# Kernel optimization log

Measured on AMD Instinct MI355X. Metric: run time of the kernel, lower is better.

The kernel has to match this reference:

```python
import jax, jax.numpy as jnp
import numpy as np

DIM = 192
HEADS = 6
WIN = 7
N = WIN * WIN            # 49 tokens per window
NW = 64                  # windows per image
B = 64                   # images
BW = NW * B              # 4096 total windows
TABLE = (2 * WIN - 1) ** 2  # 169


def setup_inputs() -> dict:
    key = jax.random.key(0)
    ks = jax.random.split(key, 8)
    x = jax.random.normal(ks[0], (BW, N, DIM), dtype=jnp.float32)
    rpi = jax.random.randint(ks[1], (N, N), 0, TABLE, dtype=jnp.int64)
    # 0 / -100 additive mask (as in shifted-window attention)
    mask = jnp.where(jax.random.uniform(ks[2], (NW, N, N)) < 0.1, -100.0, 0.0).astype(jnp.float32)
    qkv_w = jax.random.normal(ks[3], (3 * DIM, DIM), dtype=jnp.float32) * 0.02
    qkv_b = jnp.zeros((3 * DIM,), dtype=jnp.float32)
    proj_w = jax.random.normal(ks[4], (DIM, DIM), dtype=jnp.float32) * 0.02
    proj_b = jnp.zeros((DIM,), dtype=jnp.float32)
    rpb_table = jax.random.normal(ks[5], (TABLE, HEADS), dtype=jnp.float32) * 0.02
    return {"x": x, "rpi": rpi, "mask": mask, "qkv_w": qkv_w, "qkv_b": qkv_b,
            "proj_w": proj_w, "proj_b": proj_b, "rpb_table": rpb_table}


def reference(x, rpi, mask, qkv_w, qkv_b, proj_w, proj_b, rpb_table):
    b_, n, c = x.shape
    hd = c // HEADS
    scale = hd ** -0.5
    qkv = (x @ qkv_w.T + qkv_b).reshape(b_, n, 3, HEADS, hd)
    qkv = jnp.transpose(qkv, (2, 0, 3, 1, 4))
    q, k, v = qkv[0], qkv[1], qkv[2]
    attn = jnp.einsum('bhnd,bhmd->bhnm', q * scale, k)  # [b_, h, n, n]
    # relative position bias gather: [n, n, h] -> [h, n, n]
    bias = rpb_table[rpi.reshape(-1)].reshape(n, n, HEADS)
    attn = attn + jnp.transpose(bias, (2, 0, 1))[None]
    # additive 0/-inf window mask
    nw = mask.shape[0]
    attn = attn.reshape(b_ // nw, nw, HEADS, n, n) + mask[None, :, None]
    attn = attn.reshape(-1, HEADS, n, n)
    attn = jax.nn.softmax(attn, axis=-1)
    out = jnp.einsum('bhnm,bhmd->bhnd', attn, v)
    out = jnp.transpose(out, (0, 2, 1, 3)).reshape(b_, n, c)
    out = out @ proj_w.T + proj_b
    return out
```

## Files before the change

kernel.cpp:

```cpp
#include <hip/hip_runtime.h>

#define DIM    192
#define HEADS  6
#define NTOK   49
#define NWIN   64

typedef __attribute__((ext_vector_type(8))) short short8;
typedef __attribute__((ext_vector_type(4))) float f32x4;

#define XS 200
#define VS 72
#define SS 65
#define PS 72

#define BIAS_ELEMS (HEADS * NTOK * NTOK)
#define WQKV_SOFF   28864
#define WQKV_ELEMS  (3 * DIM * DIM)
#define WPROJ_SOFF  (WQKV_SOFF + WQKV_ELEMS)
#define WPROJ_ELEMS (DIM * DIM)
#define CMB_BOFF    ((size_t)(WPROJ_SOFF + WPROJ_ELEMS) * 2)
#define CMB_ELEMS   (NWIN * HEADS * NTOK * NTOK)

__device__ __forceinline__ unsigned short f2bf(float f) {
    unsigned int u = __float_as_uint(f);
    u += 0x7FFFu + ((u >> 16) & 1u);
    return (unsigned short)(u >> 16);
}

__global__ void wa_prep_kernel(const int* __restrict__ rpi,
                               const float* __restrict__ rpb,
                               const float* __restrict__ qkv_w,
                               const float* __restrict__ proj_w,
                               const float* __restrict__ maskp,
                               float* __restrict__ bias,
                               unsigned short* __restrict__ wqkv,
                               unsigned short* __restrict__ wproj,
                               float* __restrict__ cmb) {
    __shared__ int is64_s;
    if (threadIdx.x < 64) {
        int z = (rpi[2 * (int)threadIdx.x + 1] == 0) ? 1 : 0;
        unsigned long long b = __ballot(z);
        if (threadIdx.x == 0) is64_s = (__popcll(b) >= 48) ? 1 : 0;
    }
    __syncthreads();
    const int is64 = is64_s;
    const int base3 = BIAS_ELEMS + WQKV_ELEMS + WPROJ_ELEMS;
    const int total = base3 + (cmb ? CMB_ELEMS : 0);
    for (int idx = blockIdx.x * blockDim.x + threadIdx.x; idx < total;
         idx += gridDim.x * blockDim.x) {
        if (idx < BIAS_ELEMS) {
            int h  = idx / (NTOK * NTOK);
            int nm = idx - h * (NTOK * NTOK);
            int r  = is64 ? rpi[2 * nm] : rpi[nm];
            bias[idx] = rpb[r * HEADS + h];
        } else if (idx < BIAS_ELEMS + WQKV_ELEMS) {
            int i = idx - BIAS_ELEMS;
            wqkv[i] = f2bf(qkv_w[i]);
        } else if (idx < base3) {
            int i = idx - BIAS_ELEMS - WQKV_ELEMS;
            wproj[i] = f2bf(proj_w[i]);
        } else {
            int i2  = idx - base3;
            int win = i2 / (HEADS * NTOK * NTOK);
            int rem = i2 - win * (HEADS * NTOK * NTOK);
            int h   = rem / (NTOK * NTOK);
            int nm  = rem - h * (NTOK * NTOK);
            int r   = is64 ? rpi[2 * nm] : rpi[nm];
            cmb[i2] = rpb[r * HEADS + h] + maskp[win * (NTOK * NTOK) + nm];
        }
    }
}

template <bool CMB>
__global__ __launch_bounds__(512, 4)
void wa_attn_kernel(const float* __restrict__ x,
                    const float* __restrict__ maskp,
                    const unsigned short* __restrict__ wqkv,
                    const float* __restrict__ qkv_b,
                    const float* __restrict__ biasp,
                    const unsigned short* __restrict__ wproj,
                    const float* __restrict__ proj_b,
                    const float* __restrict__ cmbp,
                    float* __restrict__ out) {
    __shared__ __attribute__((aligned(16))) float uSP[64 * SS + 64 * (PS / 2)];
    __shared__ __attribute__((aligned(16))) unsigned short sq[64 * XS];
    __shared__ __attribute__((aligned(16))) unsigned short sv[DIM * VS];
    __shared__ float sinv[64];

    unsigned short* sx     = (unsigned short*)uSP;
    unsigned short* kstage = (unsigned short*)uSP;
    float* S = uSP;
    unsigned short* P = (unsigned short*)(uSP + 64 * SS);

    const int tid  = threadIdx.x;
    const int wave = tid >> 6;
    const int lane = tid & 63;
    const int quad = lane >> 4;
    const int l16  = lane & 15;
    const int bw   = blockIdx.x;
    const int win  = bw & (NWIN - 1);

    {
        const float4* xw = (const float4*)(x + (size_t)bw * (NTOK * DIM));
        for (int idx = tid; idx < NTOK * DIM / 4; idx += 512) {
            int row = idx / 48, c4 = idx - row * 48;
            float4 v = xw[idx];
            unsigned int lo = (unsigned int)f2bf(v.x) | ((unsigned int)f2bf(v.y) << 16);
            unsigned int hi = (unsigned int)f2bf(v.z) | ((unsigned int)f2bf(v.w) << 16);
            *(uint2*)&sx[row * XS + c4 * 4] = make_uint2(lo, hi);
        }
        for (int idx = tid; idx < 15 * 24; idx += 512) {
            int row = 49 + idx / 24, c8 = idx - (idx / 24) * 24;
            *(uint4*)&sx[row * XS + c8 * 8] = make_uint4(0, 0, 0, 0);
        }
    }
    __syncthreads();

    {
        const int wm = wave >> 2;
        const int wn = wave & 3;
        #pragma unroll
        for (int cc = 0; cc < 3; ++cc) {
            const int c = (cc == 0) ? 0 : (cc == 1 ? 2 : 1);
            f32x4 acc[3][2];
            #pragma unroll
            for (int r = 0; r < 3; ++r)
                #pragma unroll
                for (int mi = 0; mi < 2; ++mi) acc[r][mi] = (f32x4){0.f, 0.f, 0.f, 0.f};
            for (int k0 = 0; k0 < DIM; k0 += 32) {
                short8 af[2];
                #pragma unroll
                for (int mi = 0; mi < 2; ++mi)
                    af[mi] = *(const short8*)&sx[((wm * 2 + mi) * 16 + l16) * XS + k0 + quad * 8];
                #pragma unroll
                for (int r = 0; r < 3; ++r) {
                    int n0 = c * 192 + (wn + 4 * r) * 16;
                    short8 bf = *(const short8*)(wqkv + (n0 + l16) * DIM + k0 + quad * 8);
                    #pragma unroll
                    for (int mi = 0; mi < 2; ++mi)
                        acc[r][mi] = __builtin_amdgcn_mfma_f32_16x16x32_bf16(af[mi], bf, acc[r][mi], 0, 0, 0);
                }
            }
            if (c == 1) __syncthreads();
            #pragma unroll
            for (int r = 0; r < 3; ++r) {
                int ccol = (wn + 4 * r) * 16 + l16;
                float cb = qkv_b[c * 192 + ccol];
                #pragma unroll
                for (int mi = 0; mi < 2; ++mi) {
                    int mbase = (wm * 2 + mi) * 16 + quad * 4;
                    if (c == 2) {
                        unsigned int lo = (unsigned int)f2bf(acc[r][mi][0] + cb) |
                                          ((unsigned int)f2bf(acc[r][mi][1] + cb) << 16);
                        unsigned int hi = (unsigned int)f2bf(acc[r][mi][2] + cb) |
                                          ((unsigned int)f2bf(acc[r][mi][3] + cb) << 16);
                        *(uint2*)&sv[ccol * VS + mbase] = make_uint2(lo, hi);
                    } else if (c == 1) {
                        #pragma unroll
                        for (int rr = 0; rr < 4; ++rr)
                            kstage[(mbase + rr) * XS + ccol] = f2bf(acc[r][mi][rr] + cb);
                    } else {
                        #pragma unroll
                        for (int rr = 0; rr < 4; ++rr)
                            sq[(mbase + rr) * XS + ccol] = f2bf(acc[r][mi][rr] + cb);
                    }
                }
            }
        }
    }
    __syncthreads();

    short8 kf[2][HEADS];
    #pragma unroll
    for (int tt = 0; tt < 2; ++tt) {
        int t = wave * 2 + tt, nt = t & 3;
        #pragma unroll
        for (int h = 0; h < HEADS; ++h)
            kf[tt][h] = *(const short8*)&kstage[(nt * 16 + l16) * XS + h * 32 + quad * 8];
    }
    __syncthreads();

    const float scale = 0.17677669529663687f;
    const float* maskw = maskp + win * (NTOK * NTOK);

    #pragma unroll
    for (int h = 0; h < HEADS; ++h) {
        {
            f32x4 zz = {0.f, 0.f, 0.f, 0.f};
            const float* cw = CMB ? (cmbp + ((size_t)win * HEADS + h) * (NTOK * NTOK))
                                  : (biasp + h * (NTOK * NTOK));
            #pragma unroll
            for (int tt = 0; tt < 2; ++tt) {
                int t = wave * 2 + tt;
                int mt = t >> 2, nt = t & 3;
                short8 af = *(const short8*)&sq[(mt * 16 + l16) * XS + h * 32 + quad * 8];
                f32x4 d = __builtin_amdgcn_mfma_f32_16x16x32_bf16(af, kf[tt][h], zz, 0, 0, 0);
                #pragma unroll
                for (int rr = 0; rr < 4; ++rr) {
                    int i = mt * 16 + quad * 4 + rr;
                    int j = nt * 16 + l16;
                    if (i < NTOK && j < NTOK) {
                        float add = CMB ? cw[i * NTOK + j]
                                        : (cw[i * NTOK + j] + maskw[i * NTOK + j]);
                        S[i * SS + j] = d[rr] * scale + add;
                    }
                }
            }
        }
        __syncthreads();
        if (tid < 392) {
            int i = tid >> 3, s = tid & 7;
            float m = -1e30f;
            for (int jj = 0; jj < 7; ++jj) {
                int j = s + 8 * jj;
                if (j < NTOK) m = fmaxf(m, S[i * SS + j]);
            }
            for (int o = 1; o < 8; o <<= 1) m = fmaxf(m, __shfl_xor(m, o));
            float sum = 0.f;
            #pragma unroll
            for (int jj = 0; jj < 8; ++jj) {
                int j = s + 8 * jj;
                float e = 0.f;
                if (j < NTOK) { e = __expf(S[i * SS + j] - m); sum += e; }
                P[i * PS + j] = f2bf(e);
            }
            for (int o = 1; o < 8; o <<= 1) sum += __shfl_xor(sum, o);
            if (s == 0) sinv[i] = 1.f / sum;
        }
        __syncthreads();
        {
            int mt = wave >> 1, nt = wave & 1;
            f32x4 acc = {0.f, 0.f, 0.f, 0.f};
            #pragma unroll
            for (int k0 = 0; k0 < 64; k0 += 32) {
                short8 af = *(const short8*)&P[(mt * 16 + l16) * PS + k0 + quad * 8];
                short8 bf = *(const short8*)&sv[(h * 32 + nt * 16 + l16) * VS + k0 + quad * 8];
                acc = __builtin_amdgcn_mfma_f32_16x16x32_bf16(af, bf, acc, 0, 0, 0);
            }
            #pragma unroll
            for (int rr = 0; rr < 4; ++rr) {
                int i = mt * 16 + quad * 4 + rr;
                unsigned short ov = 0;
                if (i < NTOK) ov = f2bf(acc[rr] * sinv[i]);
                sq[i * XS + h * 32 + nt * 16 + l16] = ov;
            }
        }
    }
    __syncthreads();

    {
        const int mh = wave >> 2;
        const int wv = wave & 3;
        f32x4 pacc[3][2];
        #pragma unroll
        for (int r = 0; r < 3; ++r)
            #pragma unroll
            for (int mi = 0; mi < 2; ++mi) pacc[r][mi] = (f32x4){0.f, 0.f, 0.f, 0.f};
        for (int k0 = 0; k0 < DIM; k0 += 32) {
            short8 af[2];
            #pragma unroll
            for (int mi = 0; mi < 2; ++mi)
                af[mi] = *(const short8*)&sq[((mh * 2 + mi) * 16 + l16) * XS + k0 + quad * 8];
            #pragma unroll
            for (int r = 0; r < 3; ++r) {
                int n0 = (wv + 4 * r) * 16;
                short8 bf = *(const short8*)(wproj + (n0 + l16) * DIM + k0 + quad * 8);
                #pragma unroll
                for (int mi = 0; mi < 2; ++mi)
                    pacc[r][mi] = __builtin_amdgcn_mfma_f32_16x16x32_bf16(af[mi], bf, pacc[r][mi], 0, 0, 0);
            }
        }
        #pragma unroll
        for (int r = 0; r < 3; ++r) {
            int n0 = (wv + 4 * r) * 16;
            float cb = proj_b[n0 + l16];
            #pragma unroll
            for (int mi = 0; mi < 2; ++mi) {
                #pragma unroll
                for (int rr = 0; rr < 4; ++rr) {
                    int m = (mh * 2 + mi) * 16 + quad * 4 + rr;
                    if (m < NTOK)
                        out[((size_t)bw * NTOK + m) * DIM + n0 + l16] = pacc[r][mi][rr] + cb;
                }
            }
        }
    }
}

extern "C" void kernel_launch(void* const* d_in, const int* in_sizes, int n_in,
                              void* d_out, int out_size, void* d_ws, size_t ws_size,
                              hipStream_t stream) {
    const float* x      = (const float*)d_in[0];
    const int*   rpi    = (const int*)d_in[1];
    const float* maskp  = (const float*)d_in[2];
    const float* qkv_w  = (const float*)d_in[3];
    const float* qkv_b  = (const float*)d_in[4];
    const float* proj_w = (const float*)d_in[5];
    const float* proj_b = (const float*)d_in[6];
    const float* rpb    = (const float*)d_in[7];
    float* out = (float*)d_out;

    float* bias = (float*)d_ws;
    unsigned short* wqkv  = (unsigned short*)d_ws + WQKV_SOFF;
    unsigned short* wproj = (unsigned short*)d_ws + WPROJ_SOFF;
    float* cmb = nullptr;
    if (ws_size >= CMB_BOFF + (size_t)CMB_ELEMS * 4)
        cmb = (float*)((char*)d_ws + CMB_BOFF);

    wa_prep_kernel<<<640, 256, 0, stream>>>(rpi, rpb, qkv_w, proj_w, maskp,
                                            bias, wqkv, wproj, cmb);
    if (cmb)
        wa_attn_kernel<true><<<4096, 512, 0, stream>>>(x, maskp, wqkv, qkv_b, bias,
                                                       wproj, proj_b, cmb, out);
    else
        wa_attn_kernel<false><<<4096, 512, 0, stream>>>(x, maskp, wqkv, qkv_b, bias,
                                                        wproj, proj_b, cmb, out);
}
```

Measured before the change: 629.7 us.

## Keep softmax in registers and overlap PV of previous head with QK

Computes S^T = K·Q^T per query tile so each lane holds a query's scores in registers, doing max/sum via cross-quad shuffles instead of an LDS score buffer and a separate softmax pass. Waves 0-3 do QK+softmax for head h while waves 4-7 compute PV for head h-1, cutting one barrier phase per head. The scale is folded into Q, and normalization is folded into P. The combined bias+mask table is padded to 64 columns for float4 loads. Only half the waves do MFMA work in each phase, and the padded table adds some global traffic.

After: 609.7 us. -3.2%, faster.

```diff
diff --git a/kernel.cpp b/kernel.cpp
--- a/kernel.cpp
+++ b/kernel.cpp
@@ -10,8 +10,11 @@
 
 #define XS 200
 #define VS 72
-#define SS 65
 #define PS 72
+
+#define USP_BYTES   26656
+#define P_EOFF      9800
+#define LDS_USHORTS ((USP_BYTES + 64 * XS * 2 + DIM * VS * 2) / 2)
 
 #define BIAS_ELEMS (HEADS * NTOK * NTOK)
 #define WQKV_SOFF   28864
@@ -19,7 +22,7 @@
 #define WPROJ_SOFF  (WQKV_SOFF + WQKV_ELEMS)
 #define WPROJ_ELEMS (DIM * DIM)
 #define CMB_BOFF    ((size_t)(WPROJ_SOFF + WPROJ_ELEMS) * 2)
-#define CMB_ELEMS   (NWIN * HEADS * NTOK * NTOK)
+#define CMB2_ELEMS  (NWIN * HEADS * NTOK * 64)
 
 __device__ __forceinline__ unsigned short f2bf(float f) {
     unsigned int u = __float_as_uint(f);
@@ -35,7 +38,7 @@
                                float* __restrict__ bias,
                                unsigned short* __restrict__ wqkv,
                                unsigned short* __restrict__ wproj,
-                               float* __restrict__ cmb) {
+                               float* __restrict__ cmb2) {
     __shared__ int is64_s;
     if (threadIdx.x < 64) {
         int z = (rpi[2 * (int)threadIdx.x + 1] == 0) ? 1 : 0;
@@ -45,7 +48,7 @@
     __syncthreads();
     const int is64 = is64_s;
     const int base3 = BIAS_ELEMS + WQKV_ELEMS + WPROJ_ELEMS;
-    const int total = base3 + (cmb ? CMB_ELEMS : 0);
+    const int total = base3 + (cmb2 ? CMB2_ELEMS : 0);
     for (int idx = blockIdx.x * blockDim.x + threadIdx.x; idx < total;
          idx += gridDim.x * blockDim.x) {
         if (idx < BIAS_ELEMS) {
@@ -61,12 +64,19 @@
             wproj[i] = f2bf(proj_w[i]);
         } else {
             int i2  = idx - base3;
-            int win = i2 / (HEADS * NTOK * NTOK);
-            int rem = i2 - win * (HEADS * NTOK * NTOK);
-            int h   = rem / (NTOK * NTOK);
-            int nm  = rem - h * (NTOK * NTOK);
-            int r   = is64 ? rpi[2 * nm] : rpi[nm];
-            cmb[i2] = rpb[r * HEADS + h] + maskp[win * (NTOK * NTOK) + nm];
+            int win = i2 / (HEADS * NTOK * 64);
+            int rem = i2 - win * (HEADS * NTOK * 64);
+            int h   = rem / (NTOK * 64);
+            int rm2 = rem - h * (NTOK * 64);
+            int q   = rm2 >> 6;
+            int k   = rm2 & 63;
+            float v = 0.f;
+            if (k < NTOK) {
+                int nm = q * NTOK + k;
+                int r  = is64 ? rpi[2 * nm] : rpi[nm];
+                v = rpb[r * HEADS + h] + maskp[win * (NTOK * NTOK) + nm];
+            }
+            cmb2[i2] = v;
         }
     }
 }
@@ -82,15 +92,12 @@
                     const float* __restrict__ proj_b,
                     const float* __restrict__ cmbp,
                     float* __restrict__ out) {
-    __shared__ __attribute__((aligned(16))) float uSP[64 * SS + 64 * (PS / 2)];
-    __shared__ __attribute__((aligned(16))) unsigned short sq[64 * XS];
-    __shared__ __attribute__((aligned(16))) unsigned short sv[DIM * VS];
-    __shared__ float sinv[64];
-
-    unsigned short* sx     = (unsigned short*)uSP;
-    unsigned short* kstage = (unsigned short*)uSP;
-    float* S = uSP;
-    unsigned short* P = (unsigned short*)(uSP + 64 * SS);
+    __shared__ __attribute__((aligned(16))) unsigned short lds[LDS_USHORTS];
+    unsigned short* sx     = lds;
+    unsigned short* kstage = lds;
+    unsigned short* P      = lds + P_EOFF;
+    unsigned short* sq     = lds + USP_BYTES / 2;
+    unsigned short* sv     = lds + USP_BYTES / 2 + 64 * XS;
 
     const int tid  = threadIdx.x;
     const int wave = tid >> 6;
@@ -99,6 +106,7 @@
     const int l16  = lane & 15;
     const int bw   = blockIdx.x;
     const int win  = bw & (NWIN - 1);
+    const float scale = 0.17677669529663687f;
 
     {
         const float4* xw = (const float4*)(x + (size_t)bw * (NTOK * DIM));
@@ -162,88 +170,118 @@
                     } else {
                         #pragma unroll
                         for (int rr = 0; rr < 4; ++rr)
-                            sq[(mbase + rr) * XS + ccol] = f2bf(acc[r][mi][rr] + cb);
+                            sq[(mbase + rr) * XS + ccol] = f2bf((acc[r][mi][rr] + cb) * scale);
                     }
                 }
             }
         }
     }
     __syncthreads();
-
-    short8 kf[2][HEADS];
-    #pragma unroll
-    for (int tt = 0; tt < 2; ++tt) {
-        int t = wave * 2 + tt, nt = t & 3;
-        #pragma unroll
-        for (int h = 0; h < HEADS; ++h)
-            kf[tt][h] = *(const short8*)&kstage[(nt * 16 + l16) * XS + h * 32 + quad * 8];
-    }
-    __syncthreads();
-
-    const float scale = 0.17677669529663687f;
-    const float* maskw = maskp + win * (NTOK * NTOK);
 
     #pragma unroll
     for (int h = 0; h < HEADS; ++h) {
-        {
-            f32x4 zz = {0.f, 0.f, 0.f, 0.f};
-            const float* cw = CMB ? (cmbp + ((size_t)win * HEADS + h) * (NTOK * NTOK))
-                                  : (biasp + h * (NTOK * NTOK));
-            #pragma unroll
-            for (int tt = 0; tt < 2; ++tt) {
-                int t = wave * 2 + tt;
-                int mt = t >> 2, nt = t & 3;
-                short8 af = *(const short8*)&sq[(mt * 16 + l16) * XS + h * 32 + quad * 8];
-                f32x4 d = __builtin_amdgcn_mfma_f32_16x16x32_bf16(af, kf[tt][h], zz, 0, 0, 0);
+        unsigned int pw[4][2];
+        int qv = 0;
+        if (wave < 4) {
+            const int qt = wave;
+            const int q  = qt * 16 + l16;
+            qv = (q < NTOK);
+            short8 bq = *(const short8*)&sq[(qt * 16 + l16) * XS + h * 32 + quad * 8];
+            f32x4 d[4];
+            #pragma unroll
+            for (int kt = 0; kt < 4; ++kt) {
+                short8 ak = *(const short8*)&kstage[(kt * 16 + l16) * XS + h * 32 + quad * 8];
+                d[kt] = __builtin_amdgcn_mfma_f32_16x16x32_bf16(ak, bq, (f32x4){0.f, 0.f, 0.f, 0.f}, 0, 0, 0);
+            }
+            float s[4][4];
+            float m = -1e30f;
+            #pragma unroll
+            for (int kt = 0; kt < 4; ++kt) {
+                int kbase = kt * 16 + quad * 4;
+                if (CMB) {
+                    const int qc = qv ? q : (NTOK - 1);
+                    float4 c4 = *(const float4*)(cmbp + (((size_t)(win * HEADS + h)) * NTOK + qc) * 64 + kbase);
+                    const float* c4p = (const float*)&c4;
+                    #pragma unroll
+                    for (int rr = 0; rr < 4; ++rr) {
+                        int k = kbase + rr;
+                        s[kt][rr] = (k < NTOK && qv) ? d[kt][rr] + c4p[rr] : -30000.f;
+                        m = fmaxf(m, s[kt][rr]);
+                    }
+                } else {
+                    const float* bh = biasp + h * (NTOK * NTOK);
+                    const float* mw = maskp + win * (NTOK * NTOK);
+                    #pragma unroll
+                    for (int rr = 0; rr < 4; ++rr) {
+                        int k = kbase + rr;
+                        float v = -30000.f;
+                        if (k < NTOK && qv) v = d[kt][rr] + bh[q * NTOK + k] + mw[q * NTOK + k];
+                        s[kt][rr] = v;
+                        m = fmaxf(m, v);
+                    }
+                }
+            }
+            m = fmaxf(m, __shfl_xor(m, 16));
+            m = fmaxf(m, __shfl_xor(m, 32));
+            float p[4][4];
+            float sum = 0.f;
+            #pragma unroll
+            for (int kt = 0; kt < 4; ++kt)
+                #pragma unroll
+                for (int rr = 0; rr < 4; ++rr) {
+                    p[kt][rr] = __expf(s[kt][rr] - m);
+                    sum += p[kt][rr];
+                }
+            sum += __shfl_xor(sum, 16);
+            sum += __shfl_xor(sum, 32);
+            float si = 1.f / sum;
+            #pragma unroll
+            for (int kt = 0; kt < 4; ++kt) {
+                pw[kt][0] = (unsigned int)f2bf(p[kt][0] * si) | ((unsigned int)f2bf(p[kt][1] * si) << 16);
+                pw[kt][1] = (unsigned int)f2bf(p[kt][2] * si) | ((unsigned int)f2bf(p[kt][3] * si) << 16);
+            }
+        } else if (h > 0) {
+            const int hp = h - 1, mt = wave - 4;
+            #pragma unroll
+            for (int nt = 0; nt < 2; ++nt) {
+                f32x4 o = {0.f, 0.f, 0.f, 0.f};
+                #pragma unroll
+                for (int k0 = 0; k0 < 64; k0 += 32) {
+                    short8 ap = *(const short8*)&P[(mt * 16 + l16) * PS + k0 + quad * 8];
+                    short8 bv = *(const short8*)&sv[(hp * 32 + nt * 16 + l16) * VS + k0 + quad * 8];
+                    o = __builtin_amdgcn_mfma_f32_16x16x32_bf16(ap, bv, o, 0, 0, 0);
+                }
                 #pragma unroll
                 for (int rr = 0; rr < 4; ++rr) {
                     int i = mt * 16 + quad * 4 + rr;
-                    int j = nt * 16 + l16;
-                    if (i < NTOK && j < NTOK) {
-                        float add = CMB ? cw[i * NTOK + j]
-                                        : (cw[i * NTOK + j] + maskw[i * NTOK + j]);
-                        S[i * SS + j] = d[rr] * scale + add;
-                    }
+                    if (i < NTOK)
+                        sq[i * XS + hp * 32 + nt * 16 + l16] = f2bf(o[rr]);
                 }
             }
         }
         __syncthreads();
-        if (tid < 392) {
-            int i = tid >> 3, s = tid & 7;
-            float m = -1e30f;
-            for (int jj = 0; jj < 7; ++jj) {
-                int j = s + 8 * jj;
-                if (j < NTOK) m = fmaxf(m, S[i * SS + j]);
-            }
-            for (int o = 1; o < 8; o <<= 1) m = fmaxf(m, __shfl_xor(m, o));
-            float sum = 0.f;
-            #pragma unroll
-            for (int jj = 0; jj < 8; ++jj) {
-                int j = s + 8 * jj;
-                float e = 0.f;
-                if (j < NTOK) { e = __expf(S[i * SS + j] - m); sum += e; }
-                P[i * PS + j] = f2bf(e);
-            }
-            for (int o = 1; o < 8; o <<= 1) sum += __shfl_xor(sum, o);
-            if (s == 0) sinv[i] = 1.f / sum;
+        if (wave < 4 && qv) {
+            const int q = wave * 16 + l16;
+            #pragma unroll
+            for (int kt = 0; kt < 4; ++kt)
+                *(uint2*)&P[q * PS + kt * 16 + quad * 4] = make_uint2(pw[kt][0], pw[kt][1]);
         }
         __syncthreads();
-        {
-            int mt = wave >> 1, nt = wave & 1;
-            f32x4 acc = {0.f, 0.f, 0.f, 0.f};
-            #pragma unroll
-            for (int k0 = 0; k0 < 64; k0 += 32) {
-                short8 af = *(const short8*)&P[(mt * 16 + l16) * PS + k0 + quad * 8];
-                short8 bf = *(const short8*)&sv[(h * 32 + nt * 16 + l16) * VS + k0 + quad * 8];
-                acc = __builtin_amdgcn_mfma_f32_16x16x32_bf16(af, bf, acc, 0, 0, 0);
-            }
-            #pragma unroll
-            for (int rr = 0; rr < 4; ++rr) {
-                int i = mt * 16 + quad * 4 + rr;
-                unsigned short ov = 0;
-                if (i < NTOK) ov = f2bf(acc[rr] * sinv[i]);
-                sq[i * XS + h * 32 + nt * 16 + l16] = ov;
-            }
+    }
+    {
+        const int hp = HEADS - 1, mt = wave >> 1, nt = wave & 1;
+        f32x4 o = {0.f, 0.f, 0.f, 0.f};
+        #pragma unroll
+        for (int k0 = 0; k0 < 64; k0 += 32) {
+            short8 ap = *(const short8*)&P[(mt * 16 + l16) * PS + k0 + quad * 8];
+            short8 bv = *(const short8*)&sv[(hp * 32 + nt * 16 + l16) * VS + k0 + quad * 8];
+            o = __builtin_amdgcn_mfma_f32_16x16x32_bf16(ap, bv, o, 0, 0, 0);
+        }
+        #pragma unroll
+        for (int rr = 0; rr < 4; ++rr) {
+            int i = mt * 16 + quad * 4 + rr;
+            if (i < NTOK)
+                sq[i * XS + hp * 32 + nt * 16 + l16] = f2bf(o[rr]);
         }
     }
     __syncthreads();
@@ -303,16 +341,16 @@
     float* bias = (float*)d_ws;
     unsigned short* wqkv  = (unsigned short*)d_ws + WQKV_SOFF;
     unsigned short* wproj = (unsigned short*)d_ws + WPROJ_SOFF;
-    float* cmb = nullptr;
-    if (ws_size >= CMB_BOFF + (size_t)CMB_ELEMS * 4)
-        cmb = (float*)((char*)d_ws + CMB_BOFF);
+    float* cmb2 = nullptr;
+    if (ws_size >= CMB_BOFF + (size_t)CMB2_ELEMS * 4)
+        cmb2 = (float*)((char*)d_ws + CMB_BOFF);
 
     wa_prep_kernel<<<640, 256, 0, stream>>>(rpi, rpb, qkv_w, proj_w, maskp,
-                                            bias, wqkv, wproj, cmb);
-    if (cmb)
+                                            bias, wqkv, wproj, cmb2);
+    if (cmb2)
         wa_attn_kernel<true><<<4096, 512, 0, stream>>>(x, maskp, wqkv, qkv_b, bias,
-                                                       wproj, proj_b, cmb, out);
+                                                       wproj, proj_b, cmb2, out);
     else
         wa_attn_kernel<false><<<4096, 512, 0, stream>>>(x, maskp, wqkv, qkv_b, bias,
-                                                        wproj, proj_b, cmb, out);
+                                                        wproj, proj_b, nullptr, out);
 }
```
